# Kernel optimization log

Measured on AMD Instinct MI355X. Metric: run time of the kernel, lower is better.

Reference implementation:

```python
import jax, jax.numpy as jnp
import numpy as np

B, S, C = 32, 128, 32
VOCAB, E, H = 262, 128, 256


def _gru_dir(x_proj, mask, W_hh, b_hh, reverse):
    # x_proj: [C, N, 3H] time-major precomputed input projection
    # mask:   [C, N, 1]  1.0 where char is valid
    N = x_proj.shape[1]
    h0 = jnp.zeros((N, H), x_proj.dtype)

    def step(h, inp):
        x3, mt = inp
        gh = h @ W_hh.T + b_hh                      # [N, 3H]
        hr, hz, hn = jnp.split(gh, 3, axis=-1)
        xr, xz, xn = jnp.split(x3, 3, axis=-1)
        r = jax.nn.sigmoid(xr + hr)
        z = jax.nn.sigmoid(xz + hz)
        n = jnp.tanh(xn + r * hn)
        hnew = (1.0 - z) * n + z * h
        h = mt * hnew + (1.0 - mt) * h              # freeze state past seq end
        return h, None

    hT, _ = jax.lax.scan(step, h0, (x_proj, mask), reverse=reverse)
    return hT  # [N, H] final state at last valid step (fw) / step 0 (bw)


def char_rnn_forward(chars, chars_mask, data_mask, embed,
                     W_ih_fw, W_hh_fw, b_ih_fw, b_hh_fw,
                     W_ih_bw, W_hh_bw, b_ih_bw, b_hh_bw):
    b, s, c = chars.shape
    N = b * s
    x = embed[chars.reshape(N, c)]                      # [N, C, E]
    m = chars_mask.reshape(N, c).astype(x.dtype)        # [N, C]
    mm = jnp.moveaxis(m, 1, 0)[:, :, None]              # [C, N, 1]

    def run(W_ih, b_ih, W_hh, b_hh, reverse):
        xp = jnp.einsum('nce,ge->ncg', x, W_ih) + b_ih  # [N, C, 3H]
        xp = jnp.moveaxis(xp, 1, 0)                     # [C, N, 3H]
        return _gru_dir(xp, mm, W_hh, b_hh, reverse)

    h_fw = run(W_ih_fw, b_ih_fw, W_hh_fw, b_hh_fw, False)
    h_bw = run(W_ih_bw, b_ih_bw, W_hh_bw, b_hh_bw, True)
    final = jnp.concatenate([h_fw, h_bw], axis=-1).reshape(b, s, 2 * H)
    return final * data_mask[:, :, None].astype(final.dtype)


def setup_inputs() -> dict:
    key = jax.random.key(0)
    ks = jax.random.split(key, 16)
    chars = jax.random.randint(ks[0], (B, S, C), 0, VOCAB, dtype=jnp.int32)
    # ragged but contiguous lengths, as pack_padded_sequence assumes (>=1)
    word_len = jax.random.randint(ks[1], (B,), 1, S + 1)
    char_len = jax.random.randint(ks[2], (B, S), 1, C + 1)
    data_mask = (jnp.arange(S)[None, :] < word_len[:, None]).astype(jnp.int32)
    chars_mask = (jnp.arange(C)[None, None, :] < char_len[:, :, None]).astype(jnp.int32)
    chars_mask = chars_mask * data_mask[:, :, None]
    # pack_padded needs length>=1 even for padded words (torch never runs them;
    # we mask their output with data_mask, so give them 1 valid char)
    chars_mask = chars_mask.at[:, :, 0].set(1)

    sc = 1.0 / np.sqrt(H)
    def unif(k, shape):
        return jax.random.uniform(k, shape, jnp.float32, -sc, sc)
    embed = jax.random.normal(ks[3], (VOCAB, E), jnp.float32) * 0.1
    return {
        'chars': chars, 'chars_mask': chars_mask, 'data_mask': data_mask,
        'embed': embed,
        'W_ih_fw': unif(ks[4], (3 * H, E)), 'W_hh_fw': unif(ks[5], (3 * H, H)),
        'b_ih_fw': unif(ks[6], (3 * H,)),  'b_hh_fw': unif(ks[7], (3 * H,)),
        'W_ih_bw': unif(ks[8], (3 * H, E)), 'W_hh_bw': unif(ks[9], (3 * H, H)),
        'b_ih_bw': unif(ks[10], (3 * H,)), 'b_hh_bw': unif(ks[11], (3 * H,)),
    }


def reference(chars, chars_mask, data_mask, embed,
              W_ih_fw, W_hh_fw, b_ih_fw, b_hh_fw,
              W_ih_bw, W_hh_bw, b_ih_bw, b_hh_bw):
    return char_rnn_forward(chars, chars_mask, data_mask, embed,
                            W_ih_fw, W_hh_fw, b_ih_fw, b_hh_fw,
                            W_ih_bw, W_hh_bw, b_ih_bw, b_hh_bw)
```

## Files before the change

kernel.cpp:

```cpp
#include <hip/hip_runtime.h>
#include <hip/hip_bf16.h>

typedef unsigned int u32;
typedef unsigned short u16;
typedef __attribute__((ext_vector_type(8))) short bf16x8;
typedef __attribute__((ext_vector_type(4))) float f32x4;

#define NWORDS 4096
#define CC 32
#define EE 128
#define HHH 256
#define MMW 32
#define VOCABN 262

#define HS 264
#define XPS 784

#define PK_HHD (16*3*8*512)
#define XP_OFF_U16 (2*PK_HHD)
#define XPD (VOCABN*768)
#define BIAS_OFF_U16 (XP_OFF_U16 + 2*XPD)

#define XP_NCH 8
#define XP_CBLK ((VOCABN + XP_NCH - 1) / XP_NCH)
#define PREP_PACK_BLKS (2*PK_HHD/256)
#define PREP_XP_BLKS (XP_CBLK*2)
#define PREP_BLKS (PREP_PACK_BLKS + PREP_XP_BLKS + 1)

__device__ __forceinline__ float bf2f(u16 u){ union{u32 i; float f;} v; v.i=((u32)u)<<16; return v.f; }
__device__ __forceinline__ u16 f2bf(float f){
  __hip_bfloat16 h = __float2bfloat16(f);
  u16 r; __builtin_memcpy(&r, &h, 2); return r;
}
__device__ __forceinline__ float sigmoid_f(float x){
  float e = __builtin_amdgcn_exp2f(-1.4426950408889634f * x);
  return __builtin_amdgcn_rcpf(1.0f + e);
}
__device__ __forceinline__ float tanh_f(float x){
  float ax = __builtin_fabsf(x);
  float e  = __builtin_amdgcn_exp2f(-2.8853900817779268f * ax);
  float t  = 1.0f - 2.0f * e * __builtin_amdgcn_rcpf(1.0f + e);
  return __builtin_copysignf(t, x);
}

__global__ void prep_all(const float* __restrict__ emb,
                         const float* __restrict__ Wih_fw, const float* __restrict__ Whh_fw,
                         const float* __restrict__ bih_fw, const float* __restrict__ bhh_fw,
                         const float* __restrict__ Wih_bw, const float* __restrict__ Whh_bw,
                         const float* __restrict__ bih_bw, const float* __restrict__ bhh_bw,
                         u16* __restrict__ wsu)
{
  const int bid = blockIdx.x, tid = threadIdx.x;
  if (bid < PREP_PACK_BLKS) {
    int idx = bid*256 + tid;
    int d = idx / PK_HHD;
    int e = idx - d*PK_HHD;
    const float* Whh = d ? Whh_bw : Whh_fw;
    int jj   = e & 7;
    int lane = (e >> 3) & 63;
    int kc   = (e >> 9) & 7;
    int gnt  = e >> 12;
    int g = gnt % 3, nt = gnt / 3;
    int row = g*256 + nt*16 + (lane & 15);
    int k   = kc*32 + ((lane >> 4) << 3) + jj;
    wsu[idx] = f2bf(Whh[row*HHH + k]);
  } else if (bid < PREP_PACK_BLKS + PREP_XP_BLKS) {
    const int b    = bid - PREP_PACK_BLKS;
    const int dirb = b & 1;
    const int c0   = (b >> 1) * XP_NCH;
    const float* Wih = dirb ? Wih_bw : Wih_fw;
    u16* xpo = wsu + XP_OFF_U16 + (size_t)dirb*XPD;

    __shared__ float sh_E[XP_NCH][EE];
    for (int i = tid; i < XP_NCH*EE; i += 256) {
      int c = c0 + i/EE;
      sh_E[0][i] = (c < VOCABN) ? emb[(size_t)c*EE + (i & (EE-1))] : 0.0f;
    }
    __syncthreads();

    #pragma unroll 1
    for (int q = 0; q < 3; ++q) {
      const int g = q*256 + tid;
      const float* W = Wih + (size_t)g*EE;
      float acc[XP_NCH];
      #pragma unroll
      for (int c = 0; c < XP_NCH; ++c) acc[c] = 0.0f;
      #pragma unroll 2
      for (int k = 0; k < EE; k += 4) {
        float4 wv = *(const float4*)(W + k);
        #pragma unroll
        for (int c = 0; c < XP_NCH; ++c) {
          float4 ev = *(const float4*)(&sh_E[c][k]);
          acc[c] = fmaf(ev.w, wv.w, fmaf(ev.z, wv.z, fmaf(ev.y, wv.y, fmaf(ev.x, wv.x, acc[c]))));
        }
      }
      #pragma unroll
      for (int c = 0; c < XP_NCH; ++c) {
        int ci = c0 + c;
        if (ci < VOCABN) xpo[(size_t)ci*768 + g] = f2bf(acc[c]);
      }
    }
  } else {
    #pragma unroll
    for (int rep = 0; rep < 8; ++rep) {
      int i = rep*256 + tid;
      int d = i >> 10, o = i & 1023;
      const float* bih = d ? bih_bw : bih_fw;
      const float* bhh = d ? bhh_bw : bhh_fw;
      float v;
      if (o < 512)      v = bih[o] + bhh[o];
      else if (o < 768) v = bih[o - 512 + 512];
      else              v = bhh[o - 768 + 512];
      ((float*)(wsu + BIAS_OFF_U16))[d*1024 + o] = v;
    }
  }
}

__global__ __launch_bounds__(1024)
void gru_mfma(const int* __restrict__ chars, const int* __restrict__ chars_mask,
              const int* __restrict__ data_mask, const u16* __restrict__ wsu,
              float* __restrict__ out)
{
  const int dir   = blockIdx.x & 1;
  const int word0 = (blockIdx.x >> 1) * MMW;
  const int j     = threadIdx.x;
  const int wave  = j >> 6, lane = j & 63;
  const int quad  = lane >> 4, l15 = lane & 15;

  const bf16x8* pHH  = (const bf16x8*)(wsu + (size_t)dir*PK_HHD);
  const u16*    xpt  = wsu + XP_OFF_U16 + (size_t)dir*XPD;
  const float*  bias = (const float*)(wsu + BIAS_OFF_U16) + dir*1024;

  const bf16x8* bHH = pHH + (size_t)(wave*3)*8*64 + lane;

  __shared__ __align__(16) u16   sh_hhi[MMW][HS];
  __shared__ __align__(16) u16   sh_hlo[MMW][HS];
  __shared__ __align__(16) u16   sh_xp[MMW][XPS];
  __shared__ int   sh_ci[MMW][CC + 1];
  __shared__ float sh_cm[MMW][CC + 1];

  {
    const int w = j >> 5, c = j & 31;
    sh_ci[w][c] = chars[(word0 + w)*CC + c];
    sh_cm[w][c] = (float)chars_mask[(word0 + w)*CC + c];
  }
  for (int i = j; i < MMW*HS/2; i += 1024) { ((float*)sh_hhi)[i] = 0.0f; ((float*)sh_hlo)[i] = 0.0f; }

  const int ch = wave*16 + l15;
  const float bR  = bias[ch],        bZ  = bias[256 + ch];
  const float bXN = bias[512 + ch],  bHN = bias[768 + ch];

  const int sw = j >> 5, sp = j & 31;

  bf16x8 buf[4][3];
  auto load_batch = [&](int kc, bf16x8 dst[3]) {
    #pragma unroll
    for (int g = 0; g < 3; ++g) dst[g] = bHH[(g*8 + kc)*64];
  };
  load_batch(0, buf[0]);
  load_batch(1, buf[1]);
  load_batch(2, buf[2]);

  #pragma unroll 1
  for (int s = 0; s < CC; ++s) {
    const int t = dir ? (CC - 1 - s) : s;
    __syncthreads();
    {
      int ci = sh_ci[sw][t];
      const uint4* src = (const uint4*)(xpt + (size_t)ci*768);
      uint4 a0 = src[sp*3], a1 = src[sp*3+1], a2 = src[sp*3+2];
      *(uint4*)&sh_xp[sw][sp*24]      = a0;
      *(uint4*)&sh_xp[sw][sp*24 + 8]  = a1;
      *(uint4*)&sh_xp[sw][sp*24 + 16] = a2;
    }
    __syncthreads();

    f32x4 acc[3][2];
    #pragma unroll
    for (int m = 0; m < 2; ++m) {
      acc[0][m] = (f32x4){bR,bR,bR,bR};
      acc[1][m] = (f32x4){bZ,bZ,bZ,bZ};
      acc[2][m] = (f32x4){bHN,bHN,bHN,bHN};
    }

    auto mfma_batch = [&](int kc, bf16x8 src[3]) {
      #pragma unroll
      for (int m = 0; m < 2; ++m) {
        bf16x8 ah = *(const bf16x8*)&sh_hhi[m*16 + l15][kc*32 + quad*8];
        bf16x8 al = *(const bf16x8*)&sh_hlo[m*16 + l15][kc*32 + quad*8];
        acc[0][m] = __builtin_amdgcn_mfma_f32_16x16x32_bf16(ah, src[0], acc[0][m], 0,0,0);
        acc[1][m] = __builtin_amdgcn_mfma_f32_16x16x32_bf16(ah, src[1], acc[1][m], 0,0,0);
        acc[2][m] = __builtin_amdgcn_mfma_f32_16x16x32_bf16(ah, src[2], acc[2][m], 0,0,0);
        acc[2][m] = __builtin_amdgcn_mfma_f32_16x16x32_bf16(al, src[2], acc[2][m], 0,0,0);
      }
    };

    #pragma unroll
    for (int b = 0; b < 8; ++b) {
      mfma_batch(b, buf[b & 3]);
      load_batch((b + 3) & 7, buf[(b + 3) & 3]);
    }

    __syncthreads();

    #pragma unroll
    for (int m = 0; m < 2; ++m)
      #pragma unroll
      for (int r = 0; r < 4; ++r) {
        const int word = m*16 + quad*4 + r;
        float xr = bf2f(sh_xp[word][ch]);
        float xz = bf2f(sh_xp[word][256 + ch]);
        float xn = bf2f(sh_xp[word][512 + ch]);
        float rr = sigmoid_f(acc[0][m][r] + xr);
        float zz = sigmoid_f(acc[1][m][r] + xz);
        float nn = tanh_f(fmaf(rr, acc[2][m][r], bXN + xn));
        float hold = bf2f(sh_hhi[word][ch]) + bf2f(sh_hlo[word][ch]);
        float hnew = fmaf(zz, hold - nn, nn);
        float hm   = fmaf(sh_cm[word][t], hnew - hold, hold);
        u16 hi = f2bf(hm);
        sh_hhi[word][ch] = hi;
        sh_hlo[word][ch] = f2bf(hm - bf2f(hi));
      }
  }
  __syncthreads();

  const int oc = j & 255, og = j >> 8;
  #pragma unroll
  for (int i = 0; i < 8; ++i) {
    const int w = og*8 + i;
    float dm = (float)data_mask[word0 + w];
    float h = bf2f(sh_hhi[w][oc]) + bf2f(sh_hlo[w][oc]);
    out[(size_t)(word0 + w)*(2*HHH) + dir*HHH + oc] = h * dm;
  }
}

extern "C" void kernel_launch(void* const* d_in, const int* in_sizes, int n_in,
                              void* d_out, int out_size, void* d_ws, size_t ws_size,
                              hipStream_t stream) {
  const int*   chars      = (const int*)d_in[0];
  const int*   chars_mask = (const int*)d_in[1];
  const int*   data_mask  = (const int*)d_in[2];
  const float* embed      = (const float*)d_in[3];
  const float* Wih_fw     = (const float*)d_in[4];
  const float* Whh_fw     = (const float*)d_in[5];
  const float* bih_fw     = (const float*)d_in[6];
  const float* bhh_fw     = (const float*)d_in[7];
  const float* Wih_bw     = (const float*)d_in[8];
  const float* Whh_bw     = (const float*)d_in[9];
  const float* bih_bw     = (const float*)d_in[10];
  const float* bhh_bw     = (const float*)d_in[11];
  u16* wsu = (u16*)d_ws;

  prep_all<<<PREP_BLKS, 256, 0, stream>>>(embed, Wih_fw, Whh_fw, bih_fw, bhh_fw,
                                          Wih_bw, Whh_bw, bih_bw, bhh_bw, wsu);

  gru_mfma<<<(NWORDS/MMW)*2, 1024, 0, stream>>>(chars, chars_mask, data_mask, wsu, (float*)d_out);
}
```

Measured before the change: 366.3 us.

## Overlap xp gather with MFMA, keep hidden state in registers, coalesce weight pack

The per-step gather of input projections is now issued before the MFMA loop and written to shared memory after it. This removes one block-wide barrier per timestep and hides global load latency behind the matrix work. The fp32 hidden state is kept in registers instead of being rebuilt from the hi/lo bf16 split in shared memory. The W_hh packing prep now stages rows in shared memory and writes 16-byte vectors. The cost is more live registers (xp loads plus hreg), which could hurt occupancy.

```diff
diff --git a/kernel.cpp b/kernel.cpp
--- a/kernel.cpp
+++ b/kernel.cpp
@@ -23,7 +23,7 @@
 
 #define XP_NCH 8
 #define XP_CBLK ((VOCABN + XP_NCH - 1) / XP_NCH)
-#define PREP_PACK_BLKS (2*PK_HHD/256)
+#define PREP_PACK_BLKS 96
 #define PREP_XP_BLKS (XP_CBLK*2)
 #define PREP_BLKS (PREP_PACK_BLKS + PREP_XP_BLKS + 1)
 
@@ -52,18 +52,34 @@
 {
   const int bid = blockIdx.x, tid = threadIdx.x;
   if (bid < PREP_PACK_BLKS) {
-    int idx = bid*256 + tid;
-    int d = idx / PK_HHD;
-    int e = idx - d*PK_HHD;
+    const int d   = bid & 1;
+    const int gnt = bid >> 1;
+    const int g = gnt % 3, nt = gnt / 3;
     const float* Whh = d ? Whh_bw : Whh_fw;
-    int jj   = e & 7;
-    int lane = (e >> 3) & 63;
-    int kc   = (e >> 9) & 7;
-    int gnt  = e >> 12;
-    int g = gnt % 3, nt = gnt / 3;
-    int row = g*256 + nt*16 + (lane & 15);
-    int k   = kc*32 + ((lane >> 4) << 3) + jj;
-    wsu[idx] = f2bf(Whh[row*HHH + k]);
+    __shared__ float sh_W[16][257];
+
+    {
+      const int rr = tid >> 4, c0 = (tid & 15) * 16;
+      const float* src = Whh + (size_t)(g*256 + nt*16 + rr)*HHH + c0;
+      #pragma unroll
+      for (int i = 0; i < 16; i += 4)
+        *(float4*)&sh_W[rr][c0 + i] = *(const float4*)(src + i);
+    }
+    __syncthreads();
+    {
+      const int lane = tid & 63, kq = tid >> 6;
+      const int l15 = lane & 15, k0 = (lane >> 4) << 3;
+      #pragma unroll
+      for (int q = 0; q < 2; ++q) {
+        const int kc = kq + q*4;
+        u16 tmp[8];
+        #pragma unroll
+        for (int jj = 0; jj < 8; ++jj)
+          tmp[jj] = f2bf(sh_W[l15][kc*32 + k0 + jj]);
+        u16* dst = wsu + (size_t)d*PK_HHD + ((size_t)(gnt*8 + kc)*64 + lane)*8;
+        *(uint4*)dst = *(const uint4*)tmp;
+      }
+    }
   } else if (bid < PREP_PACK_BLKS + PREP_XP_BLKS) {
     const int b    = bid - PREP_PACK_BLKS;
     const int dirb = b & 1;
@@ -152,6 +168,12 @@
 
   const int sw = j >> 5, sp = j & 31;
 
+  float hreg[2][4];
+  #pragma unroll
+  for (int m = 0; m < 2; ++m)
+    #pragma unroll
+    for (int r = 0; r < 4; ++r) hreg[m][r] = 0.0f;
+
   bf16x8 buf[4][3];
   auto load_batch = [&](int kc, bf16x8 dst[3]) {
     #pragma unroll
@@ -165,15 +187,13 @@
   for (int s = 0; s < CC; ++s) {
     const int t = dir ? (CC - 1 - s) : s;
     __syncthreads();
+
+    uint4 a0, a1, a2;
     {
       int ci = sh_ci[sw][t];
       const uint4* src = (const uint4*)(xpt + (size_t)ci*768);
-      uint4 a0 = src[sp*3], a1 = src[sp*3+1], a2 = src[sp*3+2];
-      *(uint4*)&sh_xp[sw][sp*24]      = a0;
-      *(uint4*)&sh_xp[sw][sp*24 + 8]  = a1;
-      *(uint4*)&sh_xp[sw][sp*24 + 16] = a2;
-    }
-    __syncthreads();
+      a0 = src[sp*3]; a1 = src[sp*3+1]; a2 = src[sp*3+2];
+    }
 
     f32x4 acc[3][2];
     #pragma unroll
@@ -200,6 +220,10 @@
       mfma_batch(b, buf[b & 3]);
       load_batch((b + 3) & 7, buf[(b + 3) & 3]);
     }
+
+    *(uint4*)&sh_xp[sw][sp*24]      = a0;
+    *(uint4*)&sh_xp[sw][sp*24 + 8]  = a1;
+    *(uint4*)&sh_xp[sw][sp*24 + 16] = a2;
 
     __syncthreads();
 
@@ -214,9 +238,10 @@
         float rr = sigmoid_f(acc[0][m][r] + xr);
         float zz = sigmoid_f(acc[1][m][r] + xz);
         float nn = tanh_f(fmaf(rr, acc[2][m][r], bXN + xn));
-        float hold = bf2f(sh_hhi[word][ch]) + bf2f(sh_hlo[word][ch]);
+        float hold = hreg[m][r];
         float hnew = fmaf(zz, hold - nn, nn);
         float hm   = fmaf(sh_cm[word][t], hnew - hold, hold);
+        hreg[m][r] = hm;
         u16 hi = f2bf(hm);
         sh_hhi[word][ch] = hi;
         sh_hlo[word][ch] = f2bf(hm - bf2f(hi));
```

After: 394.0 us. 7.5% more time.
